# Kernel optimization log

Measured on AMD Instinct MI355X. Metric: run time of the kernel, lower is better.

## Reference

```python
import math
import jax, jax.numpy as jnp
import numpy as np

B, T = 64, 8192
D_OUT = 128
KPOS = 2
DT = 1.0 / 240.0


def _ema(x, alpha):
    # x: [B, T] -> causal EMA along T: acc = alpha*acc + (1-alpha)*x_t, acc0 = 0
    def step(acc, xt):
        acc = alpha * acc + (1.0 - alpha) * xt
        return acc, acc
    _, ys = jax.lax.scan(step, jnp.zeros(x.shape[0], x.dtype), x.T)  # ys: [T, B]
    return ys.T


def _fourier_axis(coord, logw, phi):
    # coord: [B,T]; logw, phi: [K] -> [B,T,2K]
    w = jnp.exp(logw)[None, None, :]
    arg = 2.0 * math.pi * coord[..., None] * w + phi[None, None, :]
    return jnp.concatenate([jnp.sin(arg), jnp.cos(arg)], axis=-1)


def setup_inputs() -> dict:
    key = jax.random.key(0)
    ks = jax.random.split(key, 4)
    gaze_xy = jax.random.normal(ks[0], (B, T, 2), dtype=jnp.float32) * 5.0
    D_in = 4 * KPOS + 12  # 20
    # xavier-uniform style init for the two Linear layers
    lim1 = math.sqrt(6.0 / (D_in + D_OUT))
    lim2 = math.sqrt(6.0 / (D_OUT + D_OUT))
    W1 = jax.random.uniform(ks[1], (D_in, D_OUT), jnp.float32, -lim1, lim1)
    b1 = jnp.zeros((D_OUT,), jnp.float32)
    W2 = jax.random.uniform(ks[2], (D_OUT, D_OUT), jnp.float32, -lim2, lim2)
    b2 = jnp.zeros((D_OUT,), jnp.float32)
    return {
        "gaze_xy": gaze_xy,
        "pos_logw_x": jnp.full((KPOS,), math.log(1.0 / 64.0), jnp.float32),
        "pos_phi_x": jnp.zeros((KPOS,), jnp.float32),
        "pos_logw_y": jnp.full((KPOS,), math.log(1.0 / 64.0), jnp.float32),
        "pos_phi_y": jnp.zeros((KPOS,), jnp.float32),
        "sac_log_thr": jnp.asarray(math.log(200.0), jnp.float32),
        "sac_invT": jnp.asarray(0.05, jnp.float32),
        "W1": W1, "b1": b1, "W2": W2, "b2": b2,
    }


def reference(gaze_xy, pos_logw_x, pos_phi_x, pos_logw_y, pos_phi_y,
              sac_log_thr, sac_invT, W1, b1, W2, b2):
    dt = max(DT, 1e-6)
    eps = 1e-6
    # causal diff with first-frame prepend (diff at t=0 is zero)
    prev = jnp.concatenate([gaze_xy[:, :1], gaze_xy[:, :-1]], axis=1)
    v = (gaze_xy - prev) / dt                      # [B,T,2]
    v_prev = jnp.concatenate([v[:, :1], v[:, :-1]], axis=1)
    a = (v - v_prev) / dt                          # [B,T,2]
    speed = jnp.linalg.norm(v, axis=-1)            # [B,T]
    inv_sp = 1.0 / (speed + eps)
    dir_cos = v[..., 0] * inv_sp
    dir_sin = v[..., 1] * inv_sp
    a_par = (v * a).sum(-1) * inv_sp
    a_perp = (v[..., 0] * a[..., 1] - v[..., 1] * a[..., 0]) * inv_sp
    thr = jnp.exp(sac_log_thr)
    gate = jax.nn.sigmoid(sac_invT * (speed - thr))  # [B,T]
    q_fast = _ema(gate, 0.8)
    q_slow = _ema(gate, 0.95)
    scalars = jnp.stack([v[..., 0], v[..., 1], speed, dir_cos, dir_sin,
                         a[..., 0], a[..., 1], a_par, a_perp,
                         gate, q_fast, q_slow], axis=-1)  # [B,T,12]
    fx = _fourier_axis(gaze_xy[..., 0], pos_logw_x, pos_phi_x)  # [B,T,4]
    fy = _fourier_axis(gaze_xy[..., 1], pos_logw_y, pos_phi_y)  # [B,T,4]
    feats = jnp.concatenate([fx, fy, scalars], axis=-1)         # [B,T,20]
    h = jax.nn.gelu(feats @ W1 + b1, approximate=False)
    h = jax.nn.gelu(h @ W2 + b2, approximate=False)
    return h
```

## Files before the change

kernel.cpp:

```cpp
#include <hip/hip_runtime.h>
#include <math.h>

#define BB 64
#define TT 8192
#define NTILES 8192
#define MLP_GRID 512
#define EMA_GRID 512

typedef short short8 __attribute__((ext_vector_type(8)));
typedef float f32x4 __attribute__((ext_vector_type(4)));

__device__ __forceinline__ unsigned short f2bf(float x) {
    unsigned int u = __float_as_uint(x);
    u += 0x7fffu + ((u >> 16) & 1u);
    return (unsigned short)(u >> 16);
}

__device__ __forceinline__ float fast_gelu(float x) {
    return x / (1.0f + __expf(-1.702f * x));
}

__global__ __launch_bounds__(256) void ema_kernel(
    const float* __restrict__ gaze, const float* __restrict__ logthr,
    const float* __restrict__ invT, float* __restrict__ qf, float* __restrict__ qs)
{
    __shared__ __align__(16) float sg[1280];
    const int tid = threadIdx.x;
    const int b   = blockIdx.x >> 3;
    const int t0  = (blockIdx.x & 7) << 10;
    const float thr = __expf(logthr[0]);
    const float sT  = invT[0];
    const float2* gz = (const float2*)gaze + (size_t)b * TT;

    #pragma unroll
    for (int it = 0; it < 5; ++it) {
        int i = tid + it * 256;
        int t = t0 - 252 + i;
        float val = 0.0f;
        if (t >= 0 && t < TT) {
            float vx = 0.0f, vy = 0.0f;
            if (t > 0) {
                float2 a = gz[t], p = gz[t - 1];
                vx = (a.x - p.x) * 240.0f;
                vy = (a.y - p.y) * 240.0f;
            }
            float speed = sqrtf(vx * vx + vy * vy);
            val = 1.0f / (1.0f + __expf(-sT * (speed - thr)));
        }
        sg[i] = val;
    }
    __syncthreads();

    const float4* sg4 = (const float4*)sg;
    float Sf = 0.0f, Ss = 0.0f;
    float wf = 0.16f;
    float ws = 0.0475f;
    for (int u = 62; u >= 0; --u) {
        float4 qv = sg4[tid + u];
        float hf = fmaf(0.8f,  fmaf(0.8f,  fmaf(0.8f,  qv.x, qv.y), qv.z), qv.w);
        Sf = fmaf(wf, hf, Sf);  wf *= 0.4096f;
        float hs = fmaf(0.95f, fmaf(0.95f, fmaf(0.95f, qv.x, qv.y), qv.z), qv.w);
        Ss = fmaf(ws, hs, Ss);  ws *= 0.81450625f;
    }
    float4 r = sg4[tid + 63];
    float g0v = r.x, g1v = r.y, g2v = r.z, g3v = r.w;

    float o0 = Sf + 0.2f * g0v;
    float o1 = fmaf(0.8f,   Sf, 0.2f * fmaf(0.8f, g0v, g1v));
    float o2 = fmaf(0.64f,  Sf, 0.2f * (g2v + 0.8f * g1v + 0.64f * g0v));
    float o3 = fmaf(0.512f, Sf, 0.2f * (g3v + 0.8f * g2v + 0.64f * g1v + 0.512f * g0v));

    float p0 = Ss + 0.05f * g0v;
    float p1 = fmaf(0.95f,     Ss, 0.05f * fmaf(0.95f, g0v, g1v));
    float p2 = fmaf(0.9025f,   Ss, 0.05f * (g2v + 0.95f * g1v + 0.9025f * g0v));
    float p3 = fmaf(0.857375f, Ss, 0.05f * (g3v + 0.95f * g2v + 0.9025f * g1v + 0.857375f * g0v));

    const size_t ob = (size_t)b * TT + t0 + 4 * tid;
    *(float4*)(qf + ob) = make_float4(o0, o1, o2, o3);
    *(float4*)(qs + ob) = make_float4(p0, p1, p2, p3);
}

__global__ __launch_bounds__(256, 2) void mlp_kernel(
    const float* __restrict__ gaze,
    const float* __restrict__ lwx, const float* __restrict__ phx,
    const float* __restrict__ lwy, const float* __restrict__ phy,
    const float* __restrict__ logthr, const float* __restrict__ invT,
    const float* __restrict__ W1, const float* __restrict__ b1,
    const float* __restrict__ W2, const float* __restrict__ b2,
    const float* __restrict__ qf, const float* __restrict__ qs,
    float* __restrict__ out)
{
    __shared__ __align__(16) unsigned short sW1T[128 * 40];
    __shared__ __align__(16) unsigned short s_pool[128 * 136];

    const int tid  = threadIdx.x;
    const int wave = tid >> 6;
    const int lane = tid & 63;
    const int c    = lane & 15;
    const int q    = lane >> 4;

    if (tid < 128) {
        const int n = tid;
        #pragma unroll
        for (int k = 0; k < 40; k += 2) {
            unsigned short lo = (k < 20)     ? f2bf(W1[k * 128 + n])       : (unsigned short)0;
            unsigned short hi = (k + 1 < 20) ? f2bf(W1[(k + 1) * 128 + n]) : (unsigned short)0;
            *(unsigned int*)&sW1T[n * 40 + k] = ((unsigned int)hi << 16) | lo;
        }
    }
    #pragma unroll
    for (int it = 0; it < 32; ++it) {
        int i  = tid + it * 256;
        int n  = i & 127;
        int kp = i >> 7;
        unsigned short lo = f2bf(W2[(2 * kp) * 128 + n]);
        unsigned short hi = f2bf(W2[(2 * kp + 1) * 128 + n]);
        *(unsigned int*)&s_pool[n * 136 + 2 * kp] = ((unsigned int)hi << 16) | lo;
    }
    __syncthreads();

    short8 B2[8][4];
    #pragma unroll
    for (int j = 0; j < 8; ++j)
        #pragma unroll
        for (int s = 0; s < 4; ++s)
            B2[j][s] = *(const short8*)&s_pool[(16 * j + c) * 136 + 32 * s + 8 * q];

    float bias1[8], bias2[8];
    #pragma unroll
    for (int j = 0; j < 8; ++j) { bias1[j] = b1[16 * j + c]; bias2[j] = b2[16 * j + c]; }

    const float twopi = 6.283185307179586f;
    const float cwx0 = twopi * __expf(lwx[0]), cwx1 = twopi * __expf(lwx[1]);
    const float cwy0 = twopi * __expf(lwy[0]), cwy1 = twopi * __expf(lwy[1]);
    const float px0 = phx[0], px1 = phx[1], py0 = phy[0], py1 = phy[1];
    const float thr = __expf(logthr[0]), sT = invT[0];

    __syncthreads();

    unsigned short* h1w = s_pool + wave * (16 * 136);
    const float2* gz = (const float2*)gaze;

    for (int tile = blockIdx.x; tile < NTILES; tile += MLP_GRID) {
        const int b   = tile >> 7;
        const int t0  = (tile & 127) << 6;
        const int t   = t0 + wave * 16 + c;
        const int idx = b * TT + t;

        float2 g0 = gz[idx];
        float2 g1 = (t > 0) ? gz[idx - 1] : g0;
        float2 g2 = (t > 1) ? gz[idx - 2] : g1;
        float vx = (g0.x - g1.x) * 240.0f;
        float vy = (g0.y - g1.y) * 240.0f;
        float vpx = (g1.x - g2.x) * 240.0f;
        float vpy = (g1.y - g2.y) * 240.0f;
        float ax = (vx - vpx) * 240.0f;
        float ay = (vy - vpy) * 240.0f;
        float speed  = sqrtf(vx * vx + vy * vy);
        float inv_sp = 1.0f / (speed + 1e-6f);

        float f[8] = {0.f, 0.f, 0.f, 0.f, 0.f, 0.f, 0.f, 0.f};
        if (q == 0) {
            __sincosf(fmaf(g0.x, cwx0, px0), &f[0], &f[2]);
            __sincosf(fmaf(g0.x, cwx1, px1), &f[1], &f[3]);
            __sincosf(fmaf(g0.y, cwy0, py0), &f[4], &f[6]);
            __sincosf(fmaf(g0.y, cwy1, py1), &f[5], &f[7]);
        } else if (q == 1) {
            f[0] = vx; f[1] = vy; f[2] = speed;
            f[3] = vx * inv_sp; f[4] = vy * inv_sp;
            f[5] = ax; f[6] = ay;
            f[7] = (vx * ax + vy * ay) * inv_sp;
        } else if (q == 2) {
            f[0] = (vx * ay - vy * ax) * inv_sp;
            f[1] = 1.0f / (1.0f + __expf(-sT * (speed - thr)));
            f[2] = qf[idx];
            f[3] = qs[idx];
        }

        union { unsigned short u[8]; short8 v; } A1;
        #pragma unroll
        for (int k = 0; k < 8; ++k) A1.u[k] = f2bf(f[k]);

        #pragma unroll
        for (int j = 0; j < 8; ++j) {
            short8 B1 = *(const short8*)&sW1T[(16 * j + c) * 40 + 8 * q];
            f32x4 acc = {bias1[j], bias1[j], bias1[j], bias1[j]};
            acc = __builtin_amdgcn_mfma_f32_16x16x32_bf16(A1.v, B1, acc, 0, 0, 0);
            #pragma unroll
            for (int r = 0; r < 4; ++r)
                h1w[(4 * q + r) * 136 + 16 * j + c] = f2bf(fast_gelu(acc[r]));
        }
        asm volatile("s_waitcnt lgkmcnt(0)" ::: "memory");

        short8 A2[4];
        #pragma unroll
        for (int s = 0; s < 4; ++s)
            A2[s] = *(const short8*)&h1w[c * 136 + 32 * s + 8 * q];

        float* ob = out + (size_t)(b * TT + t0 + wave * 16) * 128 + c;
        #pragma unroll
        for (int j = 0; j < 8; ++j) {
            f32x4 acc = {bias2[j], bias2[j], bias2[j], bias2[j]};
            #pragma unroll
            for (int s = 0; s < 4; ++s)
                acc = __builtin_amdgcn_mfma_f32_16x16x32_bf16(A2[s], B2[j][s], acc, 0, 0, 0);
            #pragma unroll
            for (int r = 0; r < 4; ++r)
                __builtin_nontemporal_store(fast_gelu(acc[r]),
                                            &ob[(4 * q + r) * 128 + 16 * j]);
        }
    }
}

extern "C" void kernel_launch(void* const* d_in, const int* in_sizes, int n_in,
                              void* d_out, int out_size, void* d_ws, size_t ws_size,
                              hipStream_t stream)
{
    const float* gaze   = (const float*)d_in[0];
    const float* lwx    = (const float*)d_in[1];
    const float* phx    = (const float*)d_in[2];
    const float* lwy    = (const float*)d_in[3];
    const float* phy    = (const float*)d_in[4];
    const float* logthr = (const float*)d_in[5];
    const float* invT   = (const float*)d_in[6];
    const float* W1     = (const float*)d_in[7];
    const float* b1     = (const float*)d_in[8];
    const float* W2     = (const float*)d_in[9];
    const float* b2     = (const float*)d_in[10];
    float* out = (float*)d_out;

    float* qf = (float*)d_ws;
    float* qs = qf + BB * TT;

    ema_kernel<<<EMA_GRID, 256, 0, stream>>>(gaze, logthr, invT, qf, qs);
    mlp_kernel<<<MLP_GRID, 256, 0, stream>>>(gaze, lwx, phx, lwy, phy, logthr, invT,
                                             W1, b1, W2, b2, qf, qs, out);
}
```

Baseline: 340.3 us.

## Move W2 fragments to LDS and W1 to registers to raise occupancy

```diff
diff --git a/kernel.cpp b/kernel.cpp
--- a/kernel.cpp
+++ b/kernel.cpp
@@ -4,7 +4,7 @@
 #define BB 64
 #define TT 8192
 #define NTILES 8192
-#define MLP_GRID 512
+#define MLP_GRID 768
 #define EMA_GRID 512
 
 typedef short short8 __attribute__((ext_vector_type(8)));
@@ -16,8 +16,12 @@
     return (unsigned short)(u >> 16);
 }
 
+__device__ __forceinline__ float fast_sigmoid(float z) {
+    return __builtin_amdgcn_rcpf(1.0f + __expf(-z));
+}
+
 __device__ __forceinline__ float fast_gelu(float x) {
-    return x / (1.0f + __expf(-1.702f * x));
+    return x * fast_sigmoid(1.702f * x);
 }
 
 __global__ __launch_bounds__(256) void ema_kernel(
@@ -80,7 +84,7 @@
     *(float4*)(qs + ob) = make_float4(p0, p1, p2, p3);
 }
 
-__global__ __launch_bounds__(256, 2) void mlp_kernel(
+__global__ __launch_bounds__(256, 3) void mlp_kernel(
     const float* __restrict__ gaze,
     const float* __restrict__ lwx, const float* __restrict__ phx,
     const float* __restrict__ lwy, const float* __restrict__ phy,
@@ -90,8 +94,8 @@
     const float* __restrict__ qf, const float* __restrict__ qs,
     float* __restrict__ out)
 {
-    __shared__ __align__(16) unsigned short sW1T[128 * 40];
-    __shared__ __align__(16) unsigned short s_pool[128 * 136];
+    __shared__ __align__(16) unsigned short sW2[128 * 136];
+    __shared__ __align__(16) unsigned short sh1[4][16 * 136];
 
     const int tid  = threadIdx.x;
     const int wave = tid >> 6;
@@ -99,15 +103,6 @@
     const int c    = lane & 15;
     const int q    = lane >> 4;
 
-    if (tid < 128) {
-        const int n = tid;
-        #pragma unroll
-        for (int k = 0; k < 40; k += 2) {
-            unsigned short lo = (k < 20)     ? f2bf(W1[k * 128 + n])       : (unsigned short)0;
-            unsigned short hi = (k + 1 < 20) ? f2bf(W1[(k + 1) * 128 + n]) : (unsigned short)0;
-            *(unsigned int*)&sW1T[n * 40 + k] = ((unsigned int)hi << 16) | lo;
-        }
-    }
     #pragma unroll
     for (int it = 0; it < 32; ++it) {
         int i  = tid + it * 256;
@@ -115,16 +110,20 @@
         int kp = i >> 7;
         unsigned short lo = f2bf(W2[(2 * kp) * 128 + n]);
         unsigned short hi = f2bf(W2[(2 * kp + 1) * 128 + n]);
-        *(unsigned int*)&s_pool[n * 136 + 2 * kp] = ((unsigned int)hi << 16) | lo;
-    }
-    __syncthreads();
-
-    short8 B2[8][4];
-    #pragma unroll
-    for (int j = 0; j < 8; ++j)
-        #pragma unroll
-        for (int s = 0; s < 4; ++s)
-            B2[j][s] = *(const short8*)&s_pool[(16 * j + c) * 136 + 32 * s + 8 * q];
+        *(unsigned int*)&sW2[n * 136 + 2 * kp] = ((unsigned int)hi << 16) | lo;
+    }
+
+    short8 B1[8];
+    #pragma unroll
+    for (int j = 0; j < 8; ++j) {
+        union { unsigned short u[8]; short8 v; } tmp;
+        #pragma unroll
+        for (int u = 0; u < 8; ++u) {
+            int k = 8 * q + u;
+            tmp.u[u] = (k < 20) ? f2bf(W1[k * 128 + 16 * j + c]) : (unsigned short)0;
+        }
+        B1[j] = tmp.v;
+    }
 
     float bias1[8], bias2[8];
     #pragma unroll
@@ -138,7 +137,7 @@
 
     __syncthreads();
 
-    unsigned short* h1w = s_pool + wave * (16 * 136);
+    unsigned short* h1w = sh1[wave];
     const float2* gz = (const float2*)gaze;
 
     for (int tile = blockIdx.x; tile < NTILES; tile += MLP_GRID) {
@@ -157,7 +156,7 @@
         float ax = (vx - vpx) * 240.0f;
         float ay = (vy - vpy) * 240.0f;
         float speed  = sqrtf(vx * vx + vy * vy);
-        float inv_sp = 1.0f / (speed + 1e-6f);
+        float inv_sp = __builtin_amdgcn_rcpf(speed + 1e-6f);
 
         float f[8] = {0.f, 0.f, 0.f, 0.f, 0.f, 0.f, 0.f, 0.f};
         if (q == 0) {
@@ -172,7 +171,7 @@
             f[7] = (vx * ax + vy * ay) * inv_sp;
         } else if (q == 2) {
             f[0] = (vx * ay - vy * ax) * inv_sp;
-            f[1] = 1.0f / (1.0f + __expf(-sT * (speed - thr)));
+            f[1] = fast_sigmoid(sT * (speed - thr));
             f[2] = qf[idx];
             f[3] = qs[idx];
         }
@@ -183,9 +182,8 @@
 
         #pragma unroll
         for (int j = 0; j < 8; ++j) {
-            short8 B1 = *(const short8*)&sW1T[(16 * j + c) * 40 + 8 * q];
             f32x4 acc = {bias1[j], bias1[j], bias1[j], bias1[j]};
-            acc = __builtin_amdgcn_mfma_f32_16x16x32_bf16(A1.v, B1, acc, 0, 0, 0);
+            acc = __builtin_amdgcn_mfma_f32_16x16x32_bf16(A1.v, B1[j], acc, 0, 0, 0);
             #pragma unroll
             for (int r = 0; r < 4; ++r)
                 h1w[(4 * q + r) * 136 + 16 * j + c] = f2bf(fast_gelu(acc[r]));
@@ -202,8 +200,10 @@
         for (int j = 0; j < 8; ++j) {
             f32x4 acc = {bias2[j], bias2[j], bias2[j], bias2[j]};
             #pragma unroll
-            for (int s = 0; s < 4; ++s)
-                acc = __builtin_amdgcn_mfma_f32_16x16x32_bf16(A2[s], B2[j][s], acc, 0, 0, 0);
+            for (int s = 0; s < 4; ++s) {
+                short8 B2 = *(const short8*)&sW2[(16 * j + c) * 136 + 32 * s + 8 * q];
+                acc = __builtin_amdgcn_mfma_f32_16x16x32_bf16(A2[s], B2, acc, 0, 0, 0);
+            }
             #pragma unroll
             for (int r = 0; r < 4; ++r)
                 __builtin_nontemporal_store(fast_gelu(acc[r]),
```

Measured after the change: 335.3 us. Within noise of the previous version (-1.5%).
